# Performance work log

Hardware: AMD Instinct MI355X
Metric: run time of the kernel (lower is better)

Reference implementation:

```python
import jax, jax.numpy as jnp
import numpy as np

K = 16  # neighbors
EPS = 1e-5

def conv1x1(x, w):
    # x: (B,C,N,1), w: (O,C) -> (B,O,N,1)
    return jnp.einsum('oc,bcnw->bonw', w, x)

def batch_norm(x, gamma, beta):
    # training-mode BatchNorm2d: biased batch stats over (B,N,W)
    mean = jnp.mean(x, axis=(0, 2, 3), keepdims=True)
    var = jnp.var(x, axis=(0, 2, 3), keepdims=True)
    xn = (x - mean) * jax.lax.rsqrt(var + EPS)
    return xn * gamma[None, :, None, None] + beta[None, :, None, None]

def gelu(x):
    return jax.nn.gelu(x, approximate=False)  # torch exact GELU

def knn_idx(x, k):
    # x: (B,C,N,1) -> neighbor indices (B,N,k), no grad (detach in torch)
    feat = jnp.squeeze(x, -1).transpose(0, 2, 1)  # (B,N,C)
    sq = jnp.sum(feat * feat, axis=-1)            # (B,N)
    dist = sq[:, :, None] - 2.0 * jnp.einsum('bnc,bmc->bnm', feat, feat) + sq[:, None, :]
    _, idx = jax.lax.top_k(-dist, k)              # nearest k (B,N,k)
    return idx

def mr_conv(x, idx, w, b, gamma, beta):
    # MRConv2d: x_j = gather neighbors, aggregate max(x_j - x_i), interleave channels, 1x1 conv + BN + GELU
    B, C, N, _ = x.shape
    feat = jnp.squeeze(x, -1)  # (B,C,N)
    # x_j[b,c,n,m] = feat[b,c,idx[b,n,m]]
    x_j = jax.vmap(lambda f, i: f[:, i])(feat, idx)      # (B,C,N,k)
    agg = jnp.max(x_j - feat[:, :, :, None], axis=-1)    # (B,C,N)
    # cat([x.unsqueeze(2), x_j.unsqueeze(2)], dim=2).reshape(B, 2C, N, 1) -> interleaved channels
    h = jnp.stack([feat, agg], axis=2).reshape(B, 2 * C, N)[..., None]  # (B,2C,N,1)
    h = jnp.einsum('oc,bcnw->bonw', w, h) + b[None, :, None, None]
    return gelu(batch_norm(h, gamma, beta))

def setup_inputs() -> dict:
    key = jax.random.key(0)
    ks = jax.random.split(key, 5)
    B, C, N = 4, 192, 4096
    s = 1.0 / np.sqrt(C)
    return {
        'x': jax.random.normal(ks[0], (B, C, N, 1), jnp.float32),
        'w_fc1': jax.random.normal(ks[1], (C, C), jnp.float32) * s,
        'w_fc2': jax.random.normal(ks[2], (C, C), jnp.float32) * s,
        'w_mr': jax.random.normal(ks[3], (C, 2 * C), jnp.float32) * (1.0 / np.sqrt(2 * C)),
        'b_mr': jnp.zeros((C,), jnp.float32),
        'g0': jnp.ones((C,), jnp.float32), 'b0': jnp.zeros((C,), jnp.float32),
        'gm': jnp.ones((C,), jnp.float32), 'bm': jnp.zeros((C,), jnp.float32),
        'g1': jnp.ones((C,), jnp.float32), 'b1': jnp.zeros((C,), jnp.float32),
    }

def reference(x, w_fc1, w_fc2, w_mr, b_mr, g0, b0, gm, bm, g1, b1):
    inp = x
    h = batch_norm(conv1x1(x, w_fc1), g0, b0)
    idx = knn_idx(jax.lax.stop_gradient(h), K)
    h = mr_conv(h, idx, w_mr, b_mr, gm, bm)
    h = batch_norm(gelu(h), g1, b1)
    h = conv1x1(h, w_fc2)
    return h + inp
```

## Files before the change

### kernel.cpp

```cpp
#include <hip/hip_runtime.h>
#include <hip/hip_bf16.h>
#include <math.h>

#define BSZ 4
#define NPT 4096
#define CH  192
#define KNB 16
#define KPH 16
#define KCAND (2 * KPH)
#define NTOT ((float)(BSZ * NPT))
#define NT64 ((double)(BSZ * NPT))

typedef short short8 __attribute__((ext_vector_type(8)));
typedef float f32x4  __attribute__((ext_vector_type(4)));

__device__ __forceinline__ float gelu_exact(float x){
    return 0.5f * x * (1.0f + erff(x * 0.70710678118654752440f));
}
__device__ __forceinline__ unsigned int umin_(unsigned int a, unsigned int b){ return a < b ? a : b; }
__device__ __forceinline__ unsigned int umax_(unsigned int a, unsigned int b){ return a < b ? b : a; }
__device__ __forceinline__ unsigned int umed3_(unsigned int a, unsigned int b, unsigned int c){
    unsigned int r;
    asm("v_med3_u32 %0, %1, %2, %3" : "=v"(r) : "v"(a), "v"(b), "v"(c));
    return r;
}
__device__ __forceinline__ unsigned short bf16rnd(float v){
    unsigned int bits = __builtin_bit_cast(unsigned int, v);
    return (unsigned short)((bits + 0x7fff + ((bits >> 16) & 1)) >> 16);
}

__global__ __launch_bounds__(256) void k_fc1_f64(
    const float* __restrict__ in, const float* __restrict__ W, double* __restrict__ outd,
    double* __restrict__ s0sum, double* __restrict__ s0sq)
{
    constexpr int OT = 8, NT = 4;
    __shared__ float wtT[CH][OT];
    __shared__ double redS[4][8], redQ[4][8];
    const int tid = threadIdx.x;
    const int o0  = blockIdx.y * OT;
    const int b   = blockIdx.z;
    const int n   = blockIdx.x * (256 * NT) + tid * NT;

    for (int lin = tid; lin < CH * OT; lin += 256){
        int c = lin >> 3, o = lin & 7;
        wtT[c][o] = W[(size_t)(o0 + o) * CH + c];
    }
    __syncthreads();

    double acc[OT][NT] = {};
    const float* ip = in + (size_t)b * CH * NPT + n;
    for (int c = 0; c < CH; ++c){
        float4 x4 = *reinterpret_cast<const float4*>(ip + (size_t)c * NPT);
        double xv[NT] = {x4.x, x4.y, x4.z, x4.w};
        float4 w0 = *reinterpret_cast<const float4*>(&wtT[c][0]);
        float4 w1 = *reinterpret_cast<const float4*>(&wtT[c][4]);
        double wv[OT] = {w0.x, w0.y, w0.z, w0.w, w1.x, w1.y, w1.z, w1.w};
        #pragma unroll
        for (int oo = 0; oo < OT; ++oo)
            #pragma unroll
            for (int j = 0; j < NT; ++j)
                acc[oo][j] = fma(wv[oo], xv[j], acc[oo][j]);
    }

    double ps[OT], pq[OT];
    #pragma unroll
    for (int oo = 0; oo < OT; ++oo){
        size_t off = ((size_t)b * CH + o0 + oo) * NPT + n;
        double s = 0., q = 0.;
        #pragma unroll
        for (int j = 0; j < 4; ++j){
            double v = acc[oo][j];
            outd[off + j] = v;
            s += v; q = fma(v, v, q);
        }
        ps[oo] = s; pq[oo] = q;
    }

    #pragma unroll
    for (int oo = 0; oo < OT; ++oo){
        #pragma unroll
        for (int off = 32; off; off >>= 1){
            ps[oo] += __shfl_xor(ps[oo], off);
            pq[oo] += __shfl_xor(pq[oo], off);
        }
    }
    const int wv = tid >> 6, lane = tid & 63;
    if (lane == 0){
        #pragma unroll
        for (int oo = 0; oo < OT; ++oo){ redS[wv][oo] = ps[oo]; redQ[wv][oo] = pq[oo]; }
    }
    __syncthreads();
    if (tid < 8){
        double s = redS[0][tid] + redS[1][tid] + redS[2][tid] + redS[3][tid];
        double q = redQ[0][tid] + redQ[1][tid] + redQ[2][tid] + redQ[3][tid];
        atomicAdd(&s0sum[o0 + tid], s);
        atomicAdd(&s0sq[o0 + tid], q);
    }
}

__global__ void k_feat(
    const double* __restrict__ t1d, const float* __restrict__ g0,
    const double* __restrict__ s0sum, const double* __restrict__ s0sq,
    double* __restrict__ featT, float* __restrict__ feat32,
    unsigned short* __restrict__ featP, float* __restrict__ sqv)
{
    __shared__ double tile[32][33];
    __shared__ float sqp[32][33];
    __shared__ double scdl[CH];
    const int n0 = blockIdx.x * 32, b = blockIdx.y;
    const int tx = threadIdx.x, ty = threadIdx.y;
    const int tid = ty * 32 + tx;
    float part[4] = {0.f, 0.f, 0.f, 0.f};
    unsigned short* fpb = featP + (size_t)b * NPT * CH;

    for (int i = tid; i < CH; i += 256){
        double mean = s0sum[i] / NT64;
        double var  = s0sq[i] / NT64 - mean * mean;
        scdl[i] = (1.0 / sqrt(var + 1e-5)) * (double)g0[i];
    }
    __syncthreads();

    for (int cc = 0; cc < CH / 32; ++cc){
        const int cbase = cc * 32;
        #pragma unroll
        for (int r = 0; r < 32; r += 8){
            int c = cbase + ty + r;
            tile[ty + r][tx] = t1d[((size_t)b * CH + c) * NPT + n0 + tx] * scdl[c];
        }
        __syncthreads();
        #pragma unroll
        for (int r = 0; r < 32; r += 8){
            int n = n0 + ty + r;
            int c = cbase + tx;
            double v = tile[tx][ty + r];
            size_t o = ((size_t)b * NPT + n) * CH + c;
            featT[o] = v;
            float f = (float)v;
            feat32[o] = f;
            part[r >> 3] = fmaf(f, f, part[r >> 3]);
        }
        if (tid < 128){
            const int t_ = tid >> 6;
            const int l  = tid & 63;
            const int r_ = l & 15, g_ = l >> 4;
            const int nl = t_ * 16 + r_;
            short8 pk;
            #pragma unroll
            for (int e = 0; e < 8; ++e)
                pk[e] = (short)bf16rnd((float)tile[g_ * 8 + e][nl]);
            const int tP = blockIdx.x * 2 + t_;
            *reinterpret_cast<short8*>(fpb + (size_t)(tP * 6 + cc) * 512 + l * 8) = pk;
        }
        __syncthreads();
    }
    #pragma unroll
    for (int j = 0; j < 4; ++j) sqp[ty + 8 * j][tx] = part[j];
    __syncthreads();
    if (ty == 0){
        float s = 0.f;
        #pragma unroll 8
        for (int k = 0; k < 32; ++k) s += sqp[tx][k];
        sqv[b * NPT + n0 + tx] = s;
    }
}

__global__ __launch_bounds__(1024, 8) void k_knn_mfma(
    const unsigned short* __restrict__ featP, const float* __restrict__ sqv,
    int* __restrict__ idxh)
{
    __shared__ unsigned int mlist[16][16][17];
    const int tid  = threadIdx.x;
    const int wv   = tid >> 6;
    const int lane = tid & 63;
    const int r = lane & 15, g = lane >> 4;
    const int b    = blockIdx.y;
    const int qt   = blockIdx.x >> 1;
    const int half = blockIdx.x & 1;
    const int qs = wv >> 2, me = wv & 3;
    const int tq   = qt * 4 + qs;
    const int tm0  = half * 128 + me * 32;
    const unsigned short* fp = featP + (size_t)b * NPT * CH;

    short8 bq0, bq1, bq2, bq3, bq4, bq5;
    {
        const unsigned short* qp = fp + (size_t)tq * 3072 + lane * 8;
        bq0 = *reinterpret_cast<const short8*>(qp);
        bq1 = *reinterpret_cast<const short8*>(qp + 512);
        bq2 = *reinterpret_cast<const short8*>(qp + 1024);
        bq3 = *reinterpret_cast<const short8*>(qp + 1536);
        bq4 = *reinterpret_cast<const short8*>(qp + 2048);
        bq5 = *reinterpret_cast<const short8*>(qp + 2560);
    }

    unsigned int Q[16];
    #pragma unroll
    for (int e = 0; e < 16; ++e) Q[e] = 0xFFFFFFFFu;

    const float* sq = sqv + b * NPT;
    const unsigned short* pa = fp + (size_t)tm0 * 3072 + lane * 8;

    for (int it = 0; it < 32; ++it){
        const unsigned short* p = pa + (size_t)it * 3072;
        short8 a0 = *reinterpret_cast<const short8*>(p);
        short8 a1 = *reinterpret_cast<const short8*>(p + 512);
        short8 a2 = *reinterpret_cast<const short8*>(p + 1024);
        short8 a3 = *reinterpret_cast<const short8*>(p + 1536);
        short8 a4 = *reinterpret_cast<const short8*>(p + 2048);
        short8 a5 = *reinterpret_cast<const short8*>(p + 2560);
        const int tm = tm0 + it;
        float4 s4 = *reinterpret_cast<const float4*>(sq + tm * 16 + 4 * g);

        f32x4 acc = {0.f, 0.f, 0.f, 0.f};
        acc = __builtin_amdgcn_mfma_f32_16x16x32_bf16(a0, bq0, acc, 0, 0, 0);
        acc = __builtin_amdgcn_mfma_f32_16x16x32_bf16(a1, bq1, acc, 0, 0, 0);
        acc = __builtin_amdgcn_mfma_f32_16x16x32_bf16(a2, bq2, acc, 0, 0, 0);
        acc = __builtin_amdgcn_mfma_f32_16x16x32_bf16(a3, bq3, acc, 0, 0, 0);
        acc = __builtin_amdgcn_mfma_f32_16x16x32_bf16(a4, bq4, acc, 0, 0, 0);
        acc = __builtin_amdgcn_mfma_f32_16x16x32_bf16(a5, bq5, acc, 0, 0, 0);

        const int m0 = tm * 16 + 4 * g;
        float sa[4] = {s4.x, s4.y, s4.z, s4.w};
        #pragma unroll
        for (int u = 0; u < 4; ++u){
            float d = fmaxf(fmaf(-2.0f, acc[u], sa[u]), 0.0f);
            unsigned int k = (__builtin_bit_cast(unsigned int, d) & 0xFFFFF000u)
                           | (unsigned int)(m0 + u);
            #pragma unroll
            for (int pz = 0; pz < 8; ++pz){
                unsigned int a = Q[2 * pz], bv = Q[2 * pz + 1];
                Q[2 * pz]     = umin_(a, k);
                Q[2 * pz + 1] = umed3_(a, bv, k);
                k             = umax_(bv, k);
            }
        }
    }

    #pragma unroll 1
    for (int rd = 0; rd < 16; ++rd){
        unsigned int v = Q[0];
        v = umin_(v, (unsigned int)__shfl_xor((int)v, 16));
        v = umin_(v, (unsigned int)__shfl_xor((int)v, 32));
        bool win = (Q[0] == v);
        if (win){
            #pragma unroll
            for (int e = 0; e < 15; ++e) Q[e] = Q[e + 1];
            Q[15] = 0xFFFFFFFFu;
        }
        if (g == 0) mlist[wv][r][rd] = v;
    }
    if (g == 0) mlist[wv][r][16] = 0xFFFFFFFFu;
    __syncthreads();

    if (tid < 64){
        const int qq = tid;
        const int q2 = qq >> 4, rr = qq & 15;
        int i0 = 0, i1 = 0, i2 = 0, i3 = 0;
        int* op = idxh + ((size_t)(b * NPT + qt * 64 + qq) * 2 + half) * KPH;
        for (int rd = 0; rd < KPH; ++rd){
            unsigned int k0 = mlist[q2 * 4 + 0][rr][i0];
            unsigned int k1 = mlist[q2 * 4 + 1][rr][i1];
            unsigned int k2 = mlist[q2 * 4 + 2][rr][i2];
            unsigned int k3 = mlist[q2 * 4 + 3][rr][i3];
            unsigned int mm = umin_(umin_(k0, k1), umin_(k2, k3));
            op[rd] = (int)(mm & 0xFFFu);
            i0 += (k0 == mm); i1 += (k1 == mm); i2 += (k2 == mm); i3 += (k3 == mm);
        }
    }
}

__global__ __launch_bounds__(256) void k_refine(
    const float* __restrict__ feat32, const double* __restrict__ featT,
    const int* __restrict__ idxh, int* __restrict__ idxf)
{
    const int q = blockIdx.x * 8 + (threadIdx.x >> 5);
    const int b = blockIdx.y;
    const int sl = threadIdx.x & 31;
    const int* cl = idxh + ((size_t)b * NPT + q) * KCAND;
    const float* qv = feat32 + ((size_t)b * NPT + q) * CH;
    float qr[6];
    #pragma unroll
    for (int j = 0; j < 6; ++j) qr[j] = qv[sl + 32 * j];

    float myd = INFINITY; int mym = 0x7fffffff;
    #pragma unroll
    for (int t0 = 0; t0 < KCAND; t0 += 8){
        float pd[8]; int cm[8];
        #pragma unroll
        for (int j = 0; j < 8; ++j){
            int m = cl[t0 + j];
            cm[j] = m;
            const float* cv = feat32 + ((size_t)b * NPT + m) * CH;
            float d = 0.f;
            #pragma unroll
            for (int e = 0; e < 6; ++e){
                float dv = cv[sl + 32 * e] - qr[e];
                d = fmaf(dv, dv, d);
            }
            pd[j] = d;
        }
        #pragma unroll
        for (int j = 0; j < 8; ++j){
            float d = pd[j];
            #pragma unroll
            for (int off = 16; off; off >>= 1) d += __shfl_xor(d, off, 32);
            if (sl == t0 + j){ myd = d; mym = cm[j]; }
        }
    }

    float d16 = 0.f;
    for (int r = 0; r < KNB; ++r){
        float bv = myd; int bi = mym;
        #pragma unroll
        for (int off = 16; off; off >>= 1){
            float ov = __shfl_xor(bv, off, 32);
            int   oi = __shfl_xor(bi, off, 32);
            if (ov < bv || (ov == bv && oi < bi)){ bv = ov; bi = oi; }
        }
        if (sl == 0) idxf[((size_t)b * NPT + q) * KNB + r] = bi;
        if (mym == bi){ myd = INFINITY; mym = 0x7fffffff; }
        d16 = bv;
    }
    float b17 = myd;
    #pragma unroll
    for (int off = 16; off; off >>= 1) b17 = fminf(b17, __shfl_xor(b17, off, 32));
    int flag = (b17 - d16 < 1e-3f + 2e-4f * d16) ? 1 : 0;
    flag = __shfl(flag, 0, 32);
    if (!flag) return;

    const double* qvd = featT + ((size_t)b * NPT + q) * CH;
    double qrd[6];
    #pragma unroll
    for (int j = 0; j < 6; ++j) qrd[j] = qvd[sl + 32 * j];
    double mydd = INFINITY; int mymd = 0x7fffffff;
    for (int t = 0; t < KCAND; ++t){
        int m = cl[t];
        const double* cv = featT + ((size_t)b * NPT + m) * CH;
        double d = 0.;
        #pragma unroll
        for (int e = 0; e < 6; ++e){
            double dv = cv[sl + 32 * e] - qrd[e];
            d = fma(dv, dv, d);
        }
        #pragma unroll
        for (int off = 16; off; off >>= 1) d += __shfl_xor(d, off, 32);
        if (sl == t){ mydd = d; mymd = m; }
    }
    for (int r = 0; r < KNB; ++r){
        double bv = mydd; int bi = mymd;
        #pragma unroll
        for (int off = 16; off; off >>= 1){
            double ov = __shfl_xor(bv, off, 32);
            int    oi = __shfl_xor(bi, off, 32);
            if (ov < bv || (ov == bv && oi < bi)){ bv = ov; bi = oi; }
        }
        if (sl == 0) idxf[((size_t)b * NPT + q) * KNB + r] = bi;
        if (mymd == bi){ mydd = INFINITY; mymd = 0x7fffffff; }
    }
}

__global__ __launch_bounds__(128) void k_gather2(
    const float* __restrict__ feat32, const float* __restrict__ g0,
    const float* __restrict__ b0, const double* __restrict__ s0sum,
    const double* __restrict__ s0sq, const int* __restrict__ idx,
    float* __restrict__ hcat)
{
    __shared__ float lt[192 * 33];
    __shared__ int il[32 * KNB];
    __shared__ float shl[CH];
    const int tid = threadIdx.x;
    const int n0  = blockIdx.x * 32;
    const int cg  = blockIdx.y;
    const int b   = blockIdx.z;

    for (int i = tid; i < 32 * KNB; i += 128)
        il[i] = idx[((size_t)b * NPT + n0) * KNB + i];
    for (int i = tid; i < CH; i += 128){
        double mean = s0sum[i] / NT64;
        double var  = s0sq[i] / NT64 - mean * mean;
        double sc   = (1.0 / sqrt(var + 1e-5)) * (double)g0[i];
        shl[i] = (float)((double)b0[i] - mean * sc);
    }
    __syncthreads();

    const int nl = tid >> 2, sub = tid & 3;
    const int n  = n0 + nl;
    const float* fbase = feat32 + (size_t)b * NPT * CH;
    const float* qr = fbase + (size_t)n * CH + cg * 96;

    float4 qv[6], mx[6];
    #pragma unroll
    for (int j = 0; j < 6; ++j){
        qv[j] = *reinterpret_cast<const float4*>(qr + (sub + 4 * j) * 4);
        mx[j] = make_float4(-INFINITY, -INFINITY, -INFINITY, -INFINITY);
    }

    #pragma unroll 4
    for (int k = 0; k < KNB; ++k){
        const float* cr = fbase + (size_t)il[nl * KNB + k] * CH + cg * 96;
        #pragma unroll
        for (int j = 0; j < 6; ++j){
            float4 v = *reinterpret_cast<const float4*>(cr + (sub + 4 * j) * 4);
            mx[j].x = fmaxf(mx[j].x, v.x - qv[j].x);
            mx[j].y = fmaxf(mx[j].y, v.y - qv[j].y);
            mx[j].z = fmaxf(mx[j].z, v.z - qv[j].z);
            mx[j].w = fmaxf(mx[j].w, v.w - qv[j].w);
        }
    }

    #pragma unroll
    for (int j = 0; j < 6; ++j){
        const int cb = (sub + 4 * j) * 4;
        float4 s4 = *reinterpret_cast<const float4*>(&shl[cg * 96 + cb]);
        float fi[4] = {qv[j].x + s4.x, qv[j].y + s4.y, qv[j].z + s4.z, qv[j].w + s4.w};
        float mm[4] = {mx[j].x, mx[j].y, mx[j].z, mx[j].w};
        #pragma unroll
        for (int e = 0; e < 4; ++e){
            int cl = cb + e;
            lt[(2 * cl) * 33 + nl]     = fi[e];
            lt[(2 * cl + 1) * 33 + nl] = mm[e];
        }
    }
    __syncthreads();

    const int rsub = tid >> 5;
    const int ni   = tid & 31;
    for (int r0 = 0; r0 < 192; r0 += 4){
        int row = r0 + rsub;
        int ch  = cg * 192 + row;
        hcat[((size_t)b * 2 * CH + ch) * NPT + n0 + ni] = lt[row * 33 + ni];
    }
}

__global__ __launch_bounds__(256) void k_gemm_mr(
    const float* __restrict__ in, const float* __restrict__ W, const float* __restrict__ bias,
    float* __restrict__ out, float* __restrict__ s1sum, float* __restrict__ s1sq)
{
    constexpr int KDIM = 2 * CH, OT = 8, NT = 4;
    __shared__ float wtT[KDIM][OT];
    __shared__ float redS[4][8], redQ[4][8];
    const int tid = threadIdx.x;
    const int o0  = blockIdx.y * OT;
    const int b   = blockIdx.z;
    const int n   = blockIdx.x * (256 * NT) + tid * NT;

    for (int lin = tid; lin < KDIM * OT; lin += 256){
        int c = lin >> 3, o = lin & 7;
        wtT[c][o] = W[(size_t)(o0 + o) * KDIM + c];
    }
    __syncthreads();

    float acc[OT][NT] = {};
    const float* ip = in + (size_t)b * KDIM * NPT + n;
    #pragma unroll 2
    for (int c = 0; c < KDIM; ++c){
        float4 x4 = *reinterpret_cast<const float4*>(ip + (size_t)c * NPT);
        float xv[NT] = {x4.x, x4.y, x4.z, x4.w};
        float4 w0 = *reinterpret_cast<const float4*>(&wtT[c][0]);
        float4 w1 = *reinterpret_cast<const float4*>(&wtT[c][4]);
        float wv[OT] = {w0.x, w0.y, w0.z, w0.w, w1.x, w1.y, w1.z, w1.w};
        #pragma unroll
        for (int oo = 0; oo < OT; ++oo)
            #pragma unroll
            for (int j = 0; j < NT; ++j)
                acc[oo][j] = fmaf(wv[oo], xv[j], acc[oo][j]);
    }

    float ps[OT], pq[OT];
    #pragma unroll
    for (int oo = 0; oo < OT; ++oo){
        size_t off = ((size_t)b * CH + o0 + oo) * NPT + n;
        float add = bias[o0 + oo];
        float vals[4];
        float s = 0.f, q = 0.f;
        #pragma unroll
        for (int j = 0; j < 4; ++j){
            vals[j] = acc[oo][j] + add;
            s += vals[j];
            q = fmaf(vals[j], vals[j], q);
        }
        ps[oo] = s; pq[oo] = q;
        float4 o4; o4.x = vals[0]; o4.y = vals[1]; o4.z = vals[2]; o4.w = vals[3];
        *reinterpret_cast<float4*>(out + off) = o4;
    }

    #pragma unroll
    for (int oo = 0; oo < OT; ++oo){
        #pragma unroll
        for (int off = 32; off; off >>= 1){
            ps[oo] += __shfl_xor(ps[oo], off);
            pq[oo] += __shfl_xor(pq[oo], off);
        }
    }
    const int wv = tid >> 6, lane = tid & 63;
    if (lane == 0){
        #pragma unroll
        for (int oo = 0; oo < OT; ++oo){ redS[wv][oo] = ps[oo]; redQ[wv][oo] = pq[oo]; }
    }
    __syncthreads();
    if (tid < 8){
        float s = redS[0][tid] + redS[1][tid] + redS[2][tid] + redS[3][tid];
        float q = redQ[0][tid] + redQ[1][tid] + redQ[2][tid] + redQ[3][tid];
        atomicAdd(&s1sum[o0 + tid], s);
        atomicAdd(&s1sq[o0 + tid], q);
    }
}

__global__ __launch_bounds__(256) void k_u(
    const float* __restrict__ in, const float* __restrict__ s1sum, const float* __restrict__ s1sq,
    const float* __restrict__ gm, const float* __restrict__ bm,
    float* __restrict__ out, float* __restrict__ s2sum, float* __restrict__ s2sq)
{
    __shared__ float redS[4], redQ[4];
    const int c = blockIdx.y, b = blockIdx.z;
    const int n = (blockIdx.x * 256 + threadIdx.x) * 4;
    const float invn = 1.0f / NTOT;
    float mean = s1sum[c] * invn;
    float var  = s1sq[c] * invn - mean * mean;
    float rstd = rsqrtf(var + 1e-5f);
    float s = rstd * gm[c], t = bm[c] - mean * s;

    size_t i = ((size_t)b * CH + c) * NPT + n;
    float4 v = *reinterpret_cast<const float4*>(in + i);
    float4 o;
    o.x = gelu_exact(gelu_exact(fmaf(v.x, s, t)));
    o.y = gelu_exact(gelu_exact(fmaf(v.y, s, t)));
    o.z = gelu_exact(gelu_exact(fmaf(v.z, s, t)));
    o.w = gelu_exact(gelu_exact(fmaf(v.w, s, t)));
    *reinterpret_cast<float4*>(out + i) = o;

    float ps = o.x + o.y + o.z + o.w;
    float pq = fmaf(o.x, o.x, fmaf(o.y, o.y, fmaf(o.z, o.z, o.w * o.w)));
    #pragma unroll
    for (int off = 32; off; off >>= 1){
        ps += __shfl_xor(ps, off);
        pq += __shfl_xor(pq, off);
    }
    const int wv = threadIdx.x >> 6, lane = threadIdx.x & 63;
    if (lane == 0){ redS[wv] = ps; redQ[wv] = pq; }
    __syncthreads();
    if (threadIdx.x == 0){
        atomicAdd(&s2sum[c], redS[0] + redS[1] + redS[2] + redS[3]);
        atomicAdd(&s2sq[c],  redQ[0] + redQ[1] + redQ[2] + redQ[3]);
    }
}

__global__ __launch_bounds__(256) void k_gemm_fc2(
    const float* __restrict__ in, const float* __restrict__ W,
    const float* __restrict__ s2sum, const float* __restrict__ s2sq,
    const float* __restrict__ g1, const float* __restrict__ b1,
    const float* __restrict__ resid, float* __restrict__ out)
{
    constexpr int KDIM = CH, OT = 8, NT = 4;
    __shared__ float wtT[KDIM][OT];
    __shared__ float scl[KDIM], shl[KDIM];
    const int tid = threadIdx.x;
    const int o0  = blockIdx.y * OT;
    const int b   = blockIdx.z;
    const int n   = blockIdx.x * (256 * NT) + tid * NT;

    for (int lin = tid; lin < KDIM * OT; lin += 256){
        int c = lin >> 3, o = lin & 7;
        wtT[c][o] = W[(size_t)(o0 + o) * KDIM + c];
    }
    const float invn = 1.0f / NTOT;
    for (int c = tid; c < KDIM; c += 256){
        float mean = s2sum[c] * invn;
        float var  = s2sq[c] * invn - mean * mean;
        float rstd = rsqrtf(var + 1e-5f);
        float s = rstd * g1[c];
        scl[c] = s;
        shl[c] = b1[c] - mean * s;
    }
    __syncthreads();

    float acc[OT][NT] = {};
    const float* ip = in + (size_t)b * KDIM * NPT + n;
    #pragma unroll 2
    for (int c = 0; c < KDIM; ++c){
        float4 x4 = *reinterpret_cast<const float4*>(ip + (size_t)c * NPT);
        float xv[NT];
        xv[0] = fmaf(x4.x, scl[c], shl[c]);
        xv[1] = fmaf(x4.y, scl[c], shl[c]);
        xv[2] = fmaf(x4.z, scl[c], shl[c]);
        xv[3] = fmaf(x4.w, scl[c], shl[c]);
        float4 w0 = *reinterpret_cast<const float4*>(&wtT[c][0]);
        float4 w1 = *reinterpret_cast<const float4*>(&wtT[c][4]);
        float wv[OT] = {w0.x, w0.y, w0.z, w0.w, w1.x, w1.y, w1.z, w1.w};
        #pragma unroll
        for (int oo = 0; oo < OT; ++oo)
            #pragma unroll
            for (int j = 0; j < NT; ++j)
                acc[oo][j] = fmaf(wv[oo], xv[j], acc[oo][j]);
    }

    #pragma unroll
    for (int oo = 0; oo < OT; ++oo){
        size_t off = ((size_t)b * CH + o0 + oo) * NPT + n;
        float4 r4 = *reinterpret_cast<const float4*>(resid + off);
        float4 o4;
        o4.x = acc[oo][0] + r4.x; o4.y = acc[oo][1] + r4.y;
        o4.z = acc[oo][2] + r4.z; o4.w = acc[oo][3] + r4.w;
        *reinterpret_cast<float4*>(out + off) = o4;
    }
}

extern "C" void kernel_launch(void* const* d_in, const int* in_sizes, int n_in,
                              void* d_out, int out_size, void* d_ws, size_t ws_size,
                              hipStream_t stream)
{
    const float* x    = (const float*)d_in[0];
    const float* w1   = (const float*)d_in[1];
    const float* w2   = (const float*)d_in[2];
    const float* wmr  = (const float*)d_in[3];
    const float* bmr  = (const float*)d_in[4];
    const float* g0   = (const float*)d_in[5];
    const float* b0   = (const float*)d_in[6];
    const float* gm   = (const float*)d_in[7];
    const float* bm   = (const float*)d_in[8];
    const float* g1   = (const float*)d_in[9];
    const float* b1   = (const float*)d_in[10];
    float* outp = (float*)d_out;

    const size_t BCN = (size_t)BSZ * CH * NPT;
    float*  A      = (float*)d_ws;
    float*  Bb     = A + BCN;
    unsigned short* featP = (unsigned short*)Bb;
    float*  Cc     = Bb + BCN;
    double* t1d    = (double*)Cc;
    double* featT  = (double*)(Cc + 2 * BCN);
    float*  feat32 = (float*)(featT + BCN);
    float*  sqv    = feat32 + BCN;
    int*    idxh   = (int*)(sqv + (size_t)BSZ * NPT);
    int*    idxf   = idxh + (size_t)BSZ * NPT * KCAND;
    float*  bnacc  = (float*)(idxf + (size_t)BSZ * NPT * KNB);
    float *s1sum = bnacc, *s1sq = bnacc + CH, *s2sum = bnacc + 2 * CH, *s2sq = bnacc + 3 * CH;
    double* s0sum  = (double*)(bnacc + 4 * CH);
    double* s0sq   = s0sum + CH;

    dim3 gg(NPT / 1024, CH / 8, BSZ);
    dim3 ge(NPT / 1024, CH, BSZ);

    hipMemsetAsync(bnacc, 0, 4 * CH * sizeof(float) + 2 * CH * sizeof(double), stream);
    k_fc1_f64<<<gg, 256, 0, stream>>>(x, w1, t1d, s0sum, s0sq);
    k_feat<<<dim3(NPT / 32, BSZ), dim3(32, 8), 0, stream>>>(t1d, g0, s0sum, s0sq,
                                                            featT, feat32, featP, sqv);
    k_knn_mfma<<<dim3(2 * NPT / 64, BSZ), 1024, 0, stream>>>(featP, sqv, idxh);
    k_refine<<<dim3(NPT / 8, BSZ), 256, 0, stream>>>(feat32, featT, idxh, idxf);
    k_gather2<<<dim3(NPT / 32, 2, BSZ), 128, 0, stream>>>(feat32, g0, b0, s0sum, s0sq, idxf, Cc);
    k_gemm_mr<<<gg, 256, 0, stream>>>(Cc, wmr, bmr, A, s1sum, s1sq);
    k_u<<<ge, 256, 0, stream>>>(A, s1sum, s1sq, gm, bm, Bb, s2sum, s2sq);
    k_gemm_fc2<<<gg, 256, 0, stream>>>(Bb, w2, s2sum, s2sq, g1, b1, x, outp);
}
```

Baseline: 372.1 us.

## Run MR conv GEMM on bf16 MFMA with fragment-packed operands from gather

The gather kernel now writes the concatenated feature/aggregate tensor directly as bf16 MFMA fragments instead of fp32 rows. A new prep kernel packs the MR weights into matching fragments. The MR GEMM is rewritten to use 16x16x32 bf16 MFMA with LDS-staged tiles and block-level BN stat accumulation. This cuts HBM traffic for the intermediate and moves the FLOPs from scalar FMA to matrix cores, at the cost of bf16 rounding of activations and weights before a BatchNorm.

```diff
diff --git a/kernel.cpp b/kernel.cpp
--- a/kernel.cpp
+++ b/kernel.cpp
@@ -362,7 +362,7 @@
     const float* __restrict__ feat32, const float* __restrict__ g0,
     const float* __restrict__ b0, const double* __restrict__ s0sum,
     const double* __restrict__ s0sq, const int* __restrict__ idx,
-    float* __restrict__ hcat)
+    unsigned short* __restrict__ hfrag)
 {
     __shared__ float lt[192 * 33];
     __shared__ int il[32 * KNB];
@@ -422,86 +422,90 @@
     }
     __syncthreads();
 
-    const int rsub = tid >> 5;
-    const int ni   = tid & 31;
-    for (int r0 = 0; r0 < 192; r0 += 4){
-        int row = r0 + rsub;
-        int ch  = cg * 192 + row;
-        hcat[((size_t)b * 2 * CH + ch) * NPT + n0 + ni] = lt[row * 33 + ni];
-    }
+    const int jt0 = (b * NPT + n0) >> 4;
+    const int wvv = tid >> 6;
+    const int l   = tid & 63;
+    for (int p = wvv; p < 12; p += 2){
+        const int t_ = p & 1, ksl = p >> 1;
+        short8 pk;
+        #pragma unroll
+        for (int e = 0; e < 8; ++e){
+            int ic = ksl * 32 + (l >> 4) * 8 + e;
+            pk[e] = (short)bf16rnd(lt[ic * 33 + t_ * 16 + (l & 15)]);
+        }
+        *reinterpret_cast<short8*>(
+            &hfrag[((size_t)(jt0 + t_) * 12 + cg * 6 + ksl) * 512 + l * 8]) = pk;
+    }
+}
+
+__global__ __launch_bounds__(64) void k_wprep(
+    const float* __restrict__ wmr, unsigned short* __restrict__ wfrag)
+{
+    const int ot = blockIdx.x, ks = blockIdx.y, l = threadIdx.x;
+    short8 pk;
+    #pragma unroll
+    for (int e = 0; e < 8; ++e)
+        pk[e] = (short)bf16rnd(wmr[(size_t)(ot * 16 + (l & 15)) * (2 * CH) + ks * 32 + (l >> 4) * 8 + e]);
+    *reinterpret_cast<short8*>(&wfrag[((size_t)ot * 12 + ks) * 512 + l * 8]) = pk;
 }
 
 __global__ __launch_bounds__(256) void k_gemm_mr(
-    const float* __restrict__ in, const float* __restrict__ W, const float* __restrict__ bias,
-    float* __restrict__ out, float* __restrict__ s1sum, float* __restrict__ s1sq)
-{
-    constexpr int KDIM = 2 * CH, OT = 8, NT = 4;
-    __shared__ float wtT[KDIM][OT];
-    __shared__ float redS[4][8], redQ[4][8];
+    const unsigned short* __restrict__ hfrag, const unsigned short* __restrict__ wfrag,
+    const float* __restrict__ bias, float* __restrict__ out,
+    float* __restrict__ s1sum, float* __restrict__ s1sq)
+{
+    __shared__ unsigned short hl[4 * 12 * 512];
+    __shared__ unsigned short wl[12 * 512];
+    __shared__ float sstat[2 * CH];
     const int tid = threadIdx.x;
-    const int o0  = blockIdx.y * OT;
-    const int b   = blockIdx.z;
-    const int n   = blockIdx.x * (256 * NT) + tid * NT;
-
-    for (int lin = tid; lin < KDIM * OT; lin += 256){
-        int c = lin >> 3, o = lin & 7;
-        wtT[c][o] = W[(size_t)(o0 + o) * KDIM + c];
-    }
-    __syncthreads();
-
-    float acc[OT][NT] = {};
-    const float* ip = in + (size_t)b * KDIM * NPT + n;
-    #pragma unroll 2
-    for (int c = 0; c < KDIM; ++c){
-        float4 x4 = *reinterpret_cast<const float4*>(ip + (size_t)c * NPT);
-        float xv[NT] = {x4.x, x4.y, x4.z, x4.w};
-        float4 w0 = *reinterpret_cast<const float4*>(&wtT[c][0]);
-        float4 w1 = *reinterpret_cast<const float4*>(&wtT[c][4]);
-        float wv[OT] = {w0.x, w0.y, w0.z, w0.w, w1.x, w1.y, w1.z, w1.w};
-        #pragma unroll
-        for (int oo = 0; oo < OT; ++oo)
-            #pragma unroll
-            for (int j = 0; j < NT; ++j)
-                acc[oo][j] = fmaf(wv[oo], xv[j], acc[oo][j]);
-    }
-
-    float ps[OT], pq[OT];
-    #pragma unroll
-    for (int oo = 0; oo < OT; ++oo){
-        size_t off = ((size_t)b * CH + o0 + oo) * NPT + n;
-        float add = bias[o0 + oo];
-        float vals[4];
-        float s = 0.f, q = 0.f;
-        #pragma unroll
-        for (int j = 0; j < 4; ++j){
-            vals[j] = acc[oo][j] + add;
-            s += vals[j];
-            q = fmaf(vals[j], vals[j], q);
-        }
-        ps[oo] = s; pq[oo] = q;
-        float4 o4; o4.x = vals[0]; o4.y = vals[1]; o4.z = vals[2]; o4.w = vals[3];
-        *reinterpret_cast<float4*>(out + off) = o4;
-    }
-
-    #pragma unroll
-    for (int oo = 0; oo < OT; ++oo){
-        #pragma unroll
-        for (int off = 32; off; off >>= 1){
-            ps[oo] += __shfl_xor(ps[oo], off);
-            pq[oo] += __shfl_xor(pq[oo], off);
-        }
-    }
     const int wv = tid >> 6, lane = tid & 63;
-    if (lane == 0){
-        #pragma unroll
-        for (int oo = 0; oo < OT; ++oo){ redS[wv][oo] = ps[oo]; redQ[wv][oo] = pq[oo]; }
-    }
-    __syncthreads();
-    if (tid < 8){
-        float s = redS[0][tid] + redS[1][tid] + redS[2][tid] + redS[3][tid];
-        float q = redQ[0][tid] + redQ[1][tid] + redQ[2][tid] + redQ[3][tid];
-        atomicAdd(&s1sum[o0 + tid], s);
-        atomicAdd(&s1sq[o0 + tid], q);
+    const int g = lane >> 4;
+    const int j0 = blockIdx.x * 64;
+    const int b  = j0 >> 12;
+    const int n0 = j0 & (NPT - 1);
+
+    const unsigned short* hsrc = hfrag + (size_t)(j0 >> 4) * 12 * 512;
+    for (int i = tid; i < 3072; i += 256)
+        *reinterpret_cast<short8*>(&hl[i * 8]) = *reinterpret_cast<const short8*>(&hsrc[i * 8]);
+    for (int i = tid; i < 2 * CH; i += 256) sstat[i] = 0.f;
+    __syncthreads();
+
+    for (int ot = 0; ot < 12; ++ot){
+        for (int i = tid; i < 768; i += 256)
+            *reinterpret_cast<short8*>(&wl[i * 8]) =
+                *reinterpret_cast<const short8*>(&wfrag[((size_t)ot * 12) * 512 + i * 8]);
+        __syncthreads();
+
+        f32x4 acc = {0.f, 0.f, 0.f, 0.f};
+        #pragma unroll
+        for (int ks = 0; ks < 12; ++ks){
+            short8 a = *reinterpret_cast<const short8*>(&wl[ks * 512 + lane * 8]);
+            short8 h = *reinterpret_cast<const short8*>(&hl[(wv * 12 + ks) * 512 + lane * 8]);
+            acc = __builtin_amdgcn_mfma_f32_16x16x32_bf16(a, h, acc, 0, 0, 0);
+        }
+
+        #pragma unroll
+        for (int u = 0; u < 4; ++u){
+            const int row = ot * 16 + 4 * g + u;
+            float val = acc[u] + bias[row];
+            out[((size_t)b * CH + row) * NPT + n0 + wv * 16 + (lane & 15)] = val;
+            float s = val, q = val * val;
+            #pragma unroll
+            for (int off = 1; off < 16; off <<= 1){
+                s += __shfl_xor(s, off, 16);
+                q += __shfl_xor(q, off, 16);
+            }
+            if ((lane & 15) == 0){
+                atomicAdd(&sstat[row], s);
+                atomicAdd(&sstat[CH + row], q);
+            }
+        }
+        __syncthreads();
+    }
+
+    if (tid < CH){
+        atomicAdd(&s1sum[tid], sstat[tid]);
+        atomicAdd(&s1sq[tid],  sstat[CH + tid]);
     }
 }
 
@@ -627,6 +631,7 @@
     unsigned short* featP = (unsigned short*)Bb;
     float*  Cc     = Bb + BCN;
     double* t1d    = (double*)Cc;
+    unsigned short* hfrag = (unsigned short*)Cc;
     double* featT  = (double*)(Cc + 2 * BCN);
     float*  feat32 = (float*)(featT + BCN);
     float*  sqv    = feat32 + BCN;
@@ -636,18 +641,20 @@
     float *s1sum = bnacc, *s1sq = bnacc + CH, *s2sum = bnacc + 2 * CH, *s2sq = bnacc + 3 * CH;
     double* s0sum  = (double*)(bnacc + 4 * CH);
     double* s0sq   = s0sum + CH;
+    unsigned short* wfrag = (unsigned short*)(s0sq + CH);
 
     dim3 gg(NPT / 1024, CH / 8, BSZ);
     dim3 ge(NPT / 1024, CH, BSZ);
 
     hipMemsetAsync(bnacc, 0, 4 * CH * sizeof(float) + 2 * CH * sizeof(double), stream);
+    k_wprep<<<dim3(12, 12), 64, 0, stream>>>(wmr, wfrag);
     k_fc1_f64<<<gg, 256, 0, stream>>>(x, w1, t1d, s0sum, s0sq);
     k_feat<<<dim3(NPT / 32, BSZ), dim3(32, 8), 0, stream>>>(t1d, g0, s0sum, s0sq,
                                                             featT, feat32, featP, sqv);
     k_knn_mfma<<<dim3(2 * NPT / 64, BSZ), 1024, 0, stream>>>(featP, sqv, idxh);
     k_refine<<<dim3(NPT / 8, BSZ), 256, 0, stream>>>(feat32, featT, idxh, idxf);
-    k_gather2<<<dim3(NPT / 32, 2, BSZ), 128, 0, stream>>>(feat32, g0, b0, s0sum, s0sq, idxf, Cc);
-    k_gemm_mr<<<gg, 256, 0, stream>>>(Cc, wmr, bmr, A, s1sum, s1sq);
+    k_gather2<<<dim3(NPT / 32, 2, BSZ), 128, 0, stream>>>(feat32, g0, b0, s0sum, s0sq, idxf, hfrag);
+    k_gemm_mr<<<dim3(BSZ * NPT / 64), 256, 0, stream>>>(hfrag, wfrag, bmr, A, s1sum, s1sq);
     k_u<<<ge, 256, 0, stream>>>(A, s1sum, s1sq, gm, bm, Bb, s2sum, s2sq);
     k_gemm_fc2<<<gg, 256, 0, stream>>>(Bb, w2, s2sum, s2sq, g1, b1, x, outp);
 }
```

Measured after the change: 336.3 us. -9.6%, faster.
